# Kernel tuning notes

Measured on AMD Instinct MI355X. Metric: run time of the kernel, lower is better.

Reference implementation:

```python
import jax, jax.numpy as jnp
import numpy as np

N_WIRES = 4
N_REUP = 3
N_Q_LAYERS = 2
SEQ_LEN = 10
GRU_HIDDEN = 16


def setup_inputs() -> dict:
    key = jax.random.key(0)
    ks = jax.random.split(key, 24)
    N, E = 10000, 320000
    s = 0.25
    inp = {
        'x': jax.random.normal(ks[0], (N, SEQ_LEN + 3), jnp.float32),
        'edge_index': jax.random.randint(ks[1], (2, E), 0, N, dtype=jnp.int32),
        'edge_attr': jax.random.normal(ks[2], (E, 1), jnp.float32),
        'W_ih': jax.random.normal(ks[3], (3 * GRU_HIDDEN, 1), jnp.float32) * s,
        'W_hh': jax.random.normal(ks[4], (3 * GRU_HIDDEN, GRU_HIDDEN), jnp.float32) * s,
        'b_ih': jax.random.normal(ks[5], (3 * GRU_HIDDEN,), jnp.float32) * s,
        'b_hh': jax.random.normal(ks[6], (3 * GRU_HIDDEN,), jnp.float32) * s,
        'p1_W': jax.random.normal(ks[7], (N_WIRES, GRU_HIDDEN + 3), jnp.float32) * s,
        'p1_b': jax.random.normal(ks[8], (N_WIRES,), jnp.float32) * s,
        'a1_W': jax.random.normal(ks[9], (1, 2 * N_WIRES), jnp.float32) * s,
        'q1_w': jax.random.uniform(ks[10], (N_REUP, N_Q_LAYERS, 2), jnp.float32, -np.pi, np.pi),
        'g1': jnp.ones((N_WIRES,), jnp.float32),
        'be1': jnp.zeros((N_WIRES,), jnp.float32),
        'p2_W': jax.random.normal(ks[11], (N_WIRES, N_WIRES), jnp.float32) * s,
        'p2_b': jax.random.normal(ks[12], (N_WIRES,), jnp.float32) * s,
        'a2_W': jax.random.normal(ks[13], (1, 2 * N_WIRES), jnp.float32) * s,
        'q2_w': jax.random.uniform(ks[14], (N_REUP, N_Q_LAYERS, 2), jnp.float32, -np.pi, np.pi),
        'g2': jnp.ones((N_WIRES,), jnp.float32),
        'be2': jnp.zeros((N_WIRES,), jnp.float32),
        'r_W': jax.random.normal(ks[15], (1, N_WIRES), jnp.float32) * s,
        'r_b': jax.random.normal(ks[16], (1,), jnp.float32) * s,
    }
    return inp


def _ry(theta):
    c = jnp.cos(theta * 0.5)
    s = jnp.sin(theta * 0.5)
    return jnp.stack([jnp.stack([c, -s], -1), jnp.stack([s, c], -1)], -2).astype(jnp.complex64)


def _rz(theta):
    em = jnp.exp(-0.5j * theta)
    ep = jnp.exp(0.5j * theta)
    z = jnp.zeros_like(em)
    return jnp.stack([jnp.stack([em, z], -1), jnp.stack([z, ep], -1)], -2)


def _apply1q(state, gate, wire):
    # state: [E,2,2,2,2]; gate: [2,2] shared or [E,2,2] per-edge
    st = jnp.moveaxis(state, 1 + wire, -1)
    if gate.ndim == 3:
        st = jnp.einsum('eij,e...j->e...i', gate, st)
    else:
        st = jnp.einsum('ij,e...j->e...i', gate, st)
    return jnp.moveaxis(st, -1, 1 + wire)


def _cnot(state, c, t):
    st = jnp.moveaxis(state, (1 + c, 1 + t), (-2, -1))
    st = jnp.concatenate([st[..., :1, :], st[..., 1:, ::-1]], axis=-2)
    return jnp.moveaxis(st, (-2, -1), (1 + c, 1 + t))


def _qcircuit(inputs, corr, weights):
    # inputs: [E,4] angles, corr: [E], weights: [3,2,2]; batched 4-wire statevector sim
    E = inputs.shape[0]
    state = jnp.zeros((E, 16), jnp.complex64).at[:, 0].set(1.0).reshape(E, 2, 2, 2, 2)
    for r in range(N_REUP):
        for i in range(N_WIRES):
            state = _apply1q(state, _ry(inputs[:, i]), i)
        state = _apply1q(state, _ry(corr), 0)
        for d in range(N_Q_LAYERS):
            gy = _ry(weights[r, d, 0])
            gz = _rz(weights[r, d, 1])
            for i in range(N_WIRES):
                state = _apply1q(state, gy, i)
                state = _apply1q(state, gz, i)
            for i in range(d % 2, N_WIRES - 1, 2):
                state = _cnot(state, i, i + 1)
    probs = state.real ** 2 + state.imag ** 2
    z = jnp.array([1.0, -1.0], jnp.float32)
    return jnp.stack(
        [jnp.einsum('e...j,j->e', jnp.moveaxis(probs, 1 + w, -1), z) for w in range(N_WIRES)], -1)


def _layernorm(x, g, b):
    mu = x.mean(-1, keepdims=True)
    v = ((x - mu) ** 2).mean(-1, keepdims=True)
    return (x - mu) * jax.lax.rsqrt(v + 1e-5) * g + b


def _qgat(x, edge_index, edge_attr, Wp, bp, Wa, qw, g, b):
    N = x.shape[0]
    h = jax.nn.elu(x @ Wp.T + bp)  # [N,4]
    sl = jnp.arange(N, dtype=edge_index.dtype)
    src = jnp.concatenate([edge_index[0], sl])
    dst = jnp.concatenate([edge_index[1], sl])
    ea = jnp.concatenate([edge_attr[:, 0], jnp.ones((N,), x.dtype)])
    alpha = jnp.concatenate([h[src], h[dst]], -1) @ Wa[0]  # [Et]
    alpha = jax.nn.leaky_relu(alpha, 0.2) * jnp.abs(ea)
    alpha = alpha - jax.lax.stop_gradient(alpha).max()
    aexp = jnp.exp(alpha)
    dsum = jax.ops.segment_sum(aexp, dst, num_segments=N)
    alpha = aexp / (dsum[dst] + 1e-8)
    corr = jnp.tanh(ea) * jnp.pi
    msg = alpha[:, None] * _qcircuit(jnp.tanh(h[src]) * jnp.pi, corr, qw)  # [Et,4]
    aggr = jax.ops.segment_sum(msg, dst, num_segments=N)
    return _layernorm(aggr + h, g, b)


def _gru_last(price_seq, W_ih, W_hh, b_ih, b_hh):
    # price_seq: [N,T] scalar-per-step GRU; returns final hidden [N,H]
    N = price_seq.shape[0]
    h0 = jnp.zeros((N, GRU_HIDDEN), price_seq.dtype)
    w_in = W_ih[:, 0]  # [3H]

    def step(h, x_t):
        gi = x_t[:, None] * w_in + b_ih  # [N,3H]
        gh = h @ W_hh.T + b_hh
        ir, iz, inn = jnp.split(gi, 3, -1)
        hr, hz, hn = jnp.split(gh, 3, -1)
        r = jax.nn.sigmoid(ir + hr)
        z = jax.nn.sigmoid(iz + hz)
        n = jnp.tanh(inn + r * hn)
        return (1.0 - z) * n + z * h, None

    h, _ = jax.lax.scan(step, h0, price_seq.T)
    return h


def reference(x, edge_index, edge_attr, W_ih, W_hh, b_ih, b_hh,
              p1_W, p1_b, a1_W, q1_w, g1, be1,
              p2_W, p2_b, a2_W, q2_w, g2, be2, r_W, r_b):
    hT = _gru_last(x[:, :SEQ_LEN], W_ih, W_hh, b_ih, b_hh)
    h = jnp.concatenate([hT, x[:, SEQ_LEN:]], -1)  # [N,19]
    h = jax.nn.relu(_qgat(h, edge_index, edge_attr, p1_W, p1_b, a1_W, q1_w, g1, be1))
    h = _qgat(h, edge_index, edge_attr, p2_W, p2_b, a2_W, q2_w, g2, be2)
    return (h @ r_W.T + r_b)[:, 0]
```

## Files before the change

### kernel.cpp

```cpp
#include <hip/hip_runtime.h>
#include <math.h>


#define GH 16
#define SEQ 10
#define PI_F 3.14159265358979323846f

__device__ __forceinline__ float sigmoidf_(float x) { return 1.0f / (1.0f + expf(-x)); }

__global__ __launch_bounds__(256) void k_gru(
    const float* __restrict__ x, const float* __restrict__ W_ih,
    const float* __restrict__ W_hh, const float* __restrict__ b_ih,
    const float* __restrict__ b_hh, const float* __restrict__ p1W,
    const float* __restrict__ p1b, const float* __restrict__ a1W,
    const int* __restrict__ ei, int* __restrict__ deg,
    float* __restrict__ nrec1, float* __restrict__ hdd1,
    float* __restrict__ Sz, int N, int E)
{
    for (int i = blockIdx.x * 256 + threadIdx.x; i < N * 10; i += gridDim.x * 256)
        Sz[i] = 0.f;
    for (int e = blockIdx.x * 256 + threadIdx.x; e < E; e += gridDim.x * 256)
        atomicAdd(&deg[ei[E + e]], 1);

    __shared__ float sW[48 * 16];
    __shared__ float sp1W[4 * 19], sp1b[4];
    for (int i = threadIdx.x; i < 48 * 16; i += 256) sW[i] = W_hh[i];
    if (threadIdx.x < 76) sp1W[threadIdx.x] = p1W[threadIdx.x];
    if (threadIdx.x < 4) sp1b[threadIdx.x] = p1b[threadIdx.x];
    __syncthreads();

    const int j = threadIdx.x & 15;
    const int n = blockIdx.x * 16 + (threadIdx.x >> 4);
    const bool valid = (n < N);

    float wr[GH], wz[GH], wn[GH];
#pragma unroll
    for (int k = 0; k < GH; ++k) {
        wr[k] = sW[j * 16 + k];
        wz[k] = sW[(16 + j) * 16 + k];
        wn[k] = sW[(32 + j) * 16 + k];
    }
    float wir = W_ih[j], wiz = W_ih[16 + j], win_ = W_ih[32 + j];
    float bir = b_ih[j], biz = b_ih[16 + j], bin_ = b_ih[32 + j];
    float brr = b_hh[j], brz = b_hh[16 + j], brn = b_hh[32 + j];

    float xv[13];
#pragma unroll
    for (int t = 0; t < 13; ++t) xv[t] = valid ? x[n * 13 + t] : 0.f;

    float h = 0.f;
#pragma unroll
    for (int t = 0; t < SEQ; ++t) {
        float xt = xv[t];
        float ghr = brr, ghz = brz, ghn = brn;
#pragma unroll
        for (int k = 0; k < GH; ++k) {
            float hk = __shfl(h, k, 16);
            ghr += wr[k] * hk; ghz += wz[k] * hk; ghn += wn[k] * hk;
        }
        float r  = sigmoidf_(xt * wir + bir + ghr);
        float z  = sigmoidf_(xt * wiz + biz + ghz);
        float nv = tanhf(xt * win_ + bin_ + r * ghn);
        h = (1.f - z) * nv + z * h;
    }

    float s0 = h * sp1W[0 * 19 + j];
    float s1 = h * sp1W[1 * 19 + j];
    float s2 = h * sp1W[2 * 19 + j];
    float s3 = h * sp1W[3 * 19 + j];
#pragma unroll
    for (int m = 1; m < 16; m <<= 1) {
        s0 += __shfl_xor(s0, m, 16);
        s1 += __shfl_xor(s1, m, 16);
        s2 += __shfl_xor(s2, m, 16);
        s3 += __shfl_xor(s3, m, 16);
    }
    if (valid && j < 4) {
        float s = (j == 0) ? s0 : (j == 1) ? s1 : (j == 2) ? s2 : s3;
        s += sp1b[j] + xv[10] * sp1W[j * 19 + 16] + xv[11] * sp1W[j * 19 + 17]
           + xv[12] * sp1W[j * 19 + 18];
        float hv = (s > 0.f) ? s : expm1f(s);
        float* nb = nrec1 + (size_t)n * 16;
        float sv, cv; sincosf(0.5f * PI_F * tanhf(hv), &sv, &cv);
        nb[2 * j]     = cv;
        nb[2 * j + 1] = sv;
        nb[12 + j]    = hv;
        float ds = hv * a1W[j];
        float dd = hv * a1W[4 + j];
        ds += __shfl_xor(ds, 1); ds += __shfl_xor(ds, 2);
        dd += __shfl_xor(dd, 1); dd += __shfl_xor(dd, 2);
        if (j == 0) { nb[8] = ds; hdd1[n] = dd; }
    }
}

__global__ __launch_bounds__(1024) void k_scan(
    const int* __restrict__ deg, int* __restrict__ off,
    int* __restrict__ cur, int N)
{
    __shared__ int part[1024];
    const int t = threadIdx.x;
    const int chunk = (N + 1023) / 1024;
    const int lo = t * chunk;
    const int hi = min(lo + chunk, N);
    int s = 0;
    for (int i = lo; i < hi; ++i) s += deg[i] + 1;
    part[t] = s;
    __syncthreads();
    for (int d = 1; d < 1024; d <<= 1) {
        int y = (t >= d) ? part[t - d] : 0;
        __syncthreads();
        part[t] += y;
        __syncthreads();
    }
    int run = part[t] - s;
    for (int i = lo; i < hi; ++i) { off[i] = run; cur[i] = run; run += deg[i] + 1; }
}

__global__ __launch_bounds__(256) void k_fill(
    const int* __restrict__ ei, const float* __restrict__ ea,
    int* __restrict__ cur, float4* __restrict__ rec, int E, int N)
{
    int idx = blockIdx.x * 256 + threadIdx.x;
    if (idx >= E + N) return;
    int src, d; float ev;
    if (idx < E) { src = ei[idx]; d = ei[E + idx]; ev = ea[idx]; }
    else         { src = idx - E; d = src;         ev = 1.0f;    }
    int slot = atomicAdd(&cur[d], 1);
    float scv, ccv; sincosf(0.5f * PI_F * tanhf(ev), &scv, &ccv);
    float4 r;
    r.x = __int_as_float(src | (d << 16));
    r.y = fabsf(ev);
    r.z = ccv; r.w = scv;
    rec[slot] = r;
}

template <int STR>
__device__ __forceinline__ void ry_g(float (&sr)[16], float (&si)[16], float c, float s) {
#pragma unroll
    for (int i0 = 0; i0 < 16; ++i0) {
        if (i0 & STR) continue;
        int i1 = i0 | STR;
        float a0r = sr[i0], a0i = si[i0], a1r = sr[i1], a1i = si[i1];
        sr[i0] = c * a0r - s * a1r; si[i0] = c * a0i - s * a1i;
        sr[i1] = s * a0r + c * a1r; si[i1] = s * a0i + c * a1i;
    }
}
template <int STR>
__device__ __forceinline__ void rz_g(float (&sr)[16], float (&si)[16], float c, float s) {
#pragma unroll
    for (int i = 0; i < 16; ++i) {
        float r = sr[i], im = si[i];
        if (i & STR) { sr[i] = r * c - im * s; si[i] = im * c + r * s; }
        else         { sr[i] = r * c + im * s; si[i] = im * c - r * s; }
    }
}
template <int SC, int ST>
__device__ __forceinline__ void cnot_g(float (&sr)[16], float (&si)[16]) {
#pragma unroll
    for (int i = 0; i < 16; ++i) {
        if ((i & SC) && !(i & ST)) {
            int j = i | ST;
            float tr = sr[i], ti = si[i];
            sr[i] = sr[j]; si[i] = si[j]; sr[j] = tr; si[j] = ti;
        }
    }
}

__global__ __launch_bounds__(128) void k_gmat(
    const float* __restrict__ q1w, const float* __restrict__ q2w,
    float* __restrict__ Gtab)
{
    int t = threadIdx.x;
    if (t >= 96) return;
    int layer = t / 48, rem = t % 48, rep = rem / 16, col = rem % 16;
    const float* qw = layer ? q2w : q1w;
    float sr[16], si[16];
#pragma unroll
    for (int i = 0; i < 16; ++i) { sr[i] = 0.f; si[i] = 0.f; }
    sr[col] = 1.f;
#pragma unroll
    for (int d = 0; d < 2; ++d) {
        float cy, sy, cz, sz;
        sincosf(0.5f * qw[(rep * 2 + d) * 2 + 0], &sy, &cy);
        sincosf(0.5f * qw[(rep * 2 + d) * 2 + 1], &sz, &cz);
        bool lastd = (rep == 2) && (d == 1);
        ry_g<8>(sr, si, cy, sy); if (!lastd) rz_g<8>(sr, si, cz, sz);
        ry_g<4>(sr, si, cy, sy); if (!lastd) rz_g<4>(sr, si, cz, sz);
        ry_g<2>(sr, si, cy, sy); if (!lastd) rz_g<2>(sr, si, cz, sz);
        ry_g<1>(sr, si, cy, sy); if (!lastd) rz_g<1>(sr, si, cz, sz);
        if (d == 0) { cnot_g<8, 4>(sr, si); cnot_g<2, 1>(sr, si); }
        else        { cnot_g<4, 2>(sr, si); }
    }
    float* g = Gtab + layer * 1536 + rep * 512;
#pragma unroll
    for (int i = 0; i < 16; ++i) {
        g[(i * 16 + col) * 2 + 0] = sr[i];
        g[(i * 16 + col) * 2 + 1] = si[i];
    }
}

__global__ __launch_bounds__(256) void k_prep(
    const float* __restrict__ nrec, const float* __restrict__ Gl,
    float* __restrict__ T, int N)
{
    __shared__ float gr[3][16 * 17], gi[3][16 * 17];
    for (int idx = threadIdx.x; idx < 3 * 256; idx += 256) {
        int rep = idx >> 8, rc = idx & 255, i = rc >> 4, jj = rc & 15;
        gr[rep][i * 17 + jj] = Gl[rep * 512 + rc * 2 + 0];
        gi[rep][i * 17 + jj] = Gl[rep * 512 + rc * 2 + 1];
    }
    __syncthreads();

    const int lane = threadIdx.x & 15;
    const int n = blockIdx.x * 16 + (threadIdx.x >> 4);
    if (n >= N) return;
    const float* nb = nrec + (size_t)n * 16;
    const float c1 = nb[2], s1 = nb[3], c2 = nb[4], s2 = nb[5], c3 = nb[6], s3 = nb[7];

    float pa = (lane & 8) ? 0.f
             : ((lane & 4) ? s1 : c1) * ((lane & 2) ? s2 : c2) * ((lane & 1) ? s3 : c3);
    float pb;
    { float t = __shfl_xor(pa, 8, 16); pb = (lane & 8) ? t : -t; }

    float ar = 0.f, ai = 0.f, br = 0.f, bi = 0.f;
#pragma unroll
    for (int jj = 0; jj < 16; ++jj) {
        float Gr = gr[0][lane * 17 + jj], Gi = gi[0][lane * 17 + jj];
        float xa = __shfl(pa, jj, 16), xb = __shfl(pb, jj, 16);
        ar += Gr * xa; ai += Gi * xa; br += Gr * xb; bi += Gi * xb;
    }

#define BFLY(vr, vi, STR, cc, ss) { \
    float tr_ = __shfl_xor(vr, STR, 16), ti_ = __shfl_xor(vi, STR, 16); \
    float sg_ = (lane & STR) ? (ss) : -(ss); \
    vr = (cc) * vr + sg_ * tr_; vi = (cc) * vi + sg_ * ti_; }
#define R123(vr, vi) { BFLY(vr, vi, 4, c1, s1) BFLY(vr, vi, 2, c2, s2) BFLY(vr, vi, 1, c3, s3) }
#define KAPP(orr, oii, xr, xi) { \
    float tr_ = __shfl_xor(xr, 8, 16), ti_ = __shfl_xor(xi, 8, 16); \
    orr = (lane & 8) ? tr_ : -tr_; oii = (lane & 8) ? ti_ : -ti_; }

    R123(ar, ai) R123(br, bi)

    float sr4[4], si4[4];
    sr4[0] = ar; si4[0] = ai;
    KAPP(sr4[1], si4[1], ar, ai)
    sr4[2] = br; si4[2] = bi;
    KAPP(sr4[3], si4[3], br, bi)

    float nr4[4] = {0.f, 0.f, 0.f, 0.f}, ni4[4] = {0.f, 0.f, 0.f, 0.f};
#pragma unroll
    for (int jj = 0; jj < 16; ++jj) {
        float Gr = gr[1][lane * 17 + jj], Gi = gi[1][lane * 17 + jj];
#pragma unroll
        for (int v = 0; v < 4; ++v) {
            float xr = __shfl(sr4[v], jj, 16), xi = __shfl(si4[v], jj, 16);
            nr4[v] += Gr * xr - Gi * xi;
            ni4[v] += Gr * xi + Gi * xr;
        }
    }
#pragma unroll
    for (int v = 0; v < 4; ++v) { R123(nr4[v], ni4[v]) }

    float gr4[4], gi4[4];
    float m01r = nr4[1] + nr4[2], m01i = ni4[1] + ni4[2];
    gr4[0] = nr4[0]; gi4[0] = ni4[0];
    { float kr, ki; KAPP(kr, ki, nr4[0], ni4[0]) gr4[1] = m01r + kr; gi4[1] = m01i + ki; }
    { float kr, ki; KAPP(kr, ki, m01r, m01i)     gr4[2] = nr4[3] + kr; gi4[2] = ni4[3] + ki; }
    { float kr, ki; KAPP(kr, ki, nr4[3], ni4[3]) gr4[3] = kr; gi4[3] = ki; }

    float vr4[4] = {0.f, 0.f, 0.f, 0.f}, vi4[4] = {0.f, 0.f, 0.f, 0.f};
#pragma unroll
    for (int jj = 0; jj < 16; ++jj) {
        float Gr = gr[2][lane * 17 + jj], Gi = gi[2][lane * 17 + jj];
#pragma unroll
        for (int v = 0; v < 4; ++v) {
            float xr = __shfl(gr4[v], jj, 16), xi = __shfl(gi4[v], jj, 16);
            vr4[v] += Gr * xr - Gi * xi;
            vi4[v] += Gr * xi + Gi * xr;
        }
    }

    float p[10];
    {
        int idx = 0;
#pragma unroll
        for (int k = 0; k < 4; ++k)
#pragma unroll
            for (int l = 0; l < 4; ++l) {
                if (l < k) continue;
                p[idx++] = vr4[k] * vr4[l] + vi4[k] * vi4[l];
            }
    }
#pragma unroll
    for (int pi = 0; pi < 10; ++pi) {
        float v = p[pi];
#pragma unroll
        for (int m = 8; m >= 1; m >>= 1) {
            float t = __shfl_xor(v, m, 16);
            v = (lane & m) ? (t - v) : (v + t);
        }
        p[pi] = v;
    }

    float* Tb = T + (size_t)n * 48;
    int w = (lane == 8) ? 0 : (lane == 4) ? 1 : (lane == 2) ? 2 : (lane == 1) ? 3 : -1;
    if (w >= 0) {
#pragma unroll
        for (int pi = 0; pi < 10; ++pi) {
            float mult = (pi == 0 || pi == 4 || pi == 7 || pi == 9) ? 1.f : 2.f;
            Tb[w * 10 + pi] = mult * p[pi];
        }
    }
    if (lane == 0) { Tb[40] = nb[0]; Tb[41] = nb[1]; Tb[42] = nb[8]; Tb[43] = 0.f; }
#undef BFLY
#undef R123
#undef KAPP
}

__device__ __forceinline__ void segreduce(
    int dst, int lane, float a0, float a1, float a2, float a3, float a4,
    float* __restrict__ S)
{
    int prevd = __shfl_up(dst, 1);
    bool head = (lane == 0) || (prevd != dst);
    unsigned long long hm = __ballot(head);
    unsigned long long below = (2ull << lane) - 1ull;
    int H = 63 - __clzll((long long)(hm & below));
    int dist = lane - H;
#pragma unroll
    for (int st = 1; st < 64; st <<= 1) {
        float t0 = __shfl_up(a0, st), t1 = __shfl_up(a1, st),
              t2 = __shfl_up(a2, st), t3 = __shfl_up(a3, st),
              t4 = __shfl_up(a4, st);
        if (dist >= st) { a0 += t0; a1 += t1; a2 += t2; a3 += t3; a4 += t4; }
    }
    int nextd = __shfl_down(dst, 1);
    bool lastl = (lane == 63) || (dst != nextd);
    if (lastl && dst >= 0) {
        float* sbase = S + (size_t)dst * 5;
        atomicAdd(sbase + 0, a0); atomicAdd(sbase + 1, a1);
        atomicAdd(sbase + 2, a2); atomicAdd(sbase + 3, a3);
        atomicAdd(sbase + 4, a4);
    }
}

__global__ __launch_bounds__(256) void k_edge(
    const float4* __restrict__ rec, const float* __restrict__ T,
    const float* __restrict__ hdd, float* __restrict__ S, int EN)
{
    const int slot = blockIdx.x * 256 + threadIdx.x;
    const int lane = threadIdx.x & 63;
    int dst = -1;
    float acc0 = 0.f, acc1 = 0.f, acc2 = 0.f, acc3 = 0.f, acc4 = 0.f;

    if (slot < EN) {
        float4 r = rec[slot];
        int ids = __float_as_int(r.x);
        int src = ids & 0xFFFF;
        dst = ids >> 16;
        float aea = r.y, ccv = r.z, scv = r.w;

        const float* Tb = T + (size_t)src * 48;
        float t[44];
#pragma unroll
        for (int q = 0; q < 11; ++q) {
            float4 v4 = *reinterpret_cast<const float4*>(Tb + q * 4);
            t[q * 4 + 0] = v4.x; t[q * 4 + 1] = v4.y;
            t[q * 4 + 2] = v4.z; t[q * 4 + 3] = v4.w;
        }
        float hdN = hdd[dst];

        float mc = t[40] * ccv - t[41] * scv;
        float ms = t[41] * ccv + t[40] * scv;
        float m2 = mc * mc, s2 = ms * ms;
        float cf0 = mc * m2, cf1 = m2 * ms, cf2 = mc * s2, cf3 = ms * s2;
        float qq[10];
        qq[0] = cf0 * cf0; qq[1] = cf0 * cf1; qq[2] = cf0 * cf2; qq[3] = cf0 * cf3;
        qq[4] = cf1 * cf1; qq[5] = cf1 * cf2; qq[6] = cf1 * cf3;
        qq[7] = cf2 * cf2; qq[8] = cf2 * cf3; qq[9] = cf3 * cf3;

        float z0 = 0.f, z1 = 0.f, z2 = 0.f, z3 = 0.f;
#pragma unroll
        for (int pi = 0; pi < 10; ++pi) {
            z0 += t[pi] * qq[pi];
            z1 += t[10 + pi] * qq[pi];
            z2 += t[20 + pi] * qq[pi];
            z3 += t[30 + pi] * qq[pi];
        }

        float s0a = t[42] + hdN;
        s0a = (s0a > 0.f) ? s0a : 0.2f * s0a;
        float aexp = expf(s0a * aea);
        acc0 = aexp * z0; acc1 = aexp * z1; acc2 = aexp * z2; acc3 = aexp * z3;
        acc4 = aexp;
    }
    segreduce(dst, lane, acc0, acc1, acc2, acc3, acc4, S);
}

template <bool FINAL>
__global__ __launch_bounds__(256) void k_node(
    const float* __restrict__ S, const float* __restrict__ nrec,
    const float* __restrict__ g4, const float* __restrict__ be4,
    const float* __restrict__ pW, const float* __restrict__ pb,
    const float* __restrict__ WaN, const float* __restrict__ rW,
    const float* __restrict__ rb, float* __restrict__ onrec,
    float* __restrict__ ohdd, float* __restrict__ out, int N)
{
    int n = blockIdx.x * 256 + threadIdx.x;
    if (n >= N) return;
    const float* sb = S + (size_t)n * 5;
    const float* nb = nrec + (size_t)n * 16;
    float dn = sb[4] + 1e-8f;
    float v0 = sb[0] / dn + nb[12];
    float v1 = sb[1] / dn + nb[13];
    float v2 = sb[2] / dn + nb[14];
    float v3 = sb[3] / dn + nb[15];
    float mu = 0.25f * (v0 + v1 + v2 + v3);
    float d0 = v0 - mu, d1 = v1 - mu, d2 = v2 - mu, d3 = v3 - mu;
    float var = 0.25f * (d0 * d0 + d1 * d1 + d2 * d2 + d3 * d3);
    float rs = 1.0f / sqrtf(var + 1e-5f);
    float y0 = d0 * rs * g4[0] + be4[0];
    float y1 = d1 * rs * g4[1] + be4[1];
    float y2 = d2 * rs * g4[2] + be4[2];
    float y3 = d3 * rs * g4[3] + be4[3];

    if (FINAL) {
        out[n] = rb[0] + y0 * rW[0] + y1 * rW[1] + y2 * rW[2] + y3 * rW[3];
    } else {
        y0 = fmaxf(y0, 0.f); y1 = fmaxf(y1, 0.f);
        y2 = fmaxf(y2, 0.f); y3 = fmaxf(y3, 0.f);
        float hv[4];
#pragma unroll
        for (int w = 0; w < 4; ++w) {
            float s = pb[w] + y0 * pW[w * 4 + 0] + y1 * pW[w * 4 + 1]
                    + y2 * pW[w * 4 + 2] + y3 * pW[w * 4 + 3];
            hv[w] = (s > 0.f) ? s : expm1f(s);
        }
        float* ob = onrec + (size_t)n * 16;
        float ds = 0.f, dd = 0.f;
#pragma unroll
        for (int w = 0; w < 4; ++w) {
            float sv, cv; sincosf(0.5f * PI_F * tanhf(hv[w]), &sv, &cv);
            ob[2 * w]     = cv;
            ob[2 * w + 1] = sv;
            ob[12 + w]    = hv[w];
            ds += hv[w] * WaN[w];
            dd += hv[w] * WaN[4 + w];
        }
        ob[8] = ds;
        ohdd[n] = dd;
    }
}

extern "C" void kernel_launch(void* const* d_in, const int* in_sizes, int n_in,
                              void* d_out, int out_size, void* d_ws, size_t ws_size,
                              hipStream_t stream)
{
    const float* x    = (const float*)d_in[0];
    const int*   ei   = (const int*)d_in[1];
    const float* ea   = (const float*)d_in[2];
    const float* W_ih = (const float*)d_in[3];
    const float* W_hh = (const float*)d_in[4];
    const float* b_ih = (const float*)d_in[5];
    const float* b_hh = (const float*)d_in[6];
    const float* p1W  = (const float*)d_in[7];
    const float* p1b  = (const float*)d_in[8];
    const float* a1W  = (const float*)d_in[9];
    const float* q1w  = (const float*)d_in[10];
    const float* g1   = (const float*)d_in[11];
    const float* be1  = (const float*)d_in[12];
    const float* p2W  = (const float*)d_in[13];
    const float* p2b  = (const float*)d_in[14];
    const float* a2W  = (const float*)d_in[15];
    const float* q2w  = (const float*)d_in[16];
    const float* g2   = (const float*)d_in[17];
    const float* be2  = (const float*)d_in[18];
    const float* rW   = (const float*)d_in[19];
    const float* rb   = (const float*)d_in[20];
    float* out = (float*)d_out;

    int N  = in_sizes[0] / 13;
    int E  = in_sizes[1] / 2;
    int EN = E + N;

    float* ws    = (float*)d_ws;
    float* nrec1 = ws;
    float* nrec2 = nrec1 + (size_t)N * 16;
    float* hdd1  = nrec2 + (size_t)N * 16;
    float* hdd2  = hdd1 + N;
    float* S1    = hdd2 + N;
    float* S2    = S1 + (size_t)N * 5;
    float* Gtab  = S2 + (size_t)N * 5;
    float* T     = Gtab + 3072;
    int* deg  = (int*)(T + (size_t)N * 48);
    int* off  = deg + N;
    int* cur  = off + N;
    uintptr_t rp = (uintptr_t)(cur + N);
    rp = (rp + 15u) & ~(uintptr_t)15u;
    float4* rec = (float4*)rp;

    hipMemsetAsync(deg, 0, (size_t)N * sizeof(int), stream);

    const int B = 256;
    k_gru<<<(N + 15) / 16, B, 0, stream>>>(x, W_ih, W_hh, b_ih, b_hh, p1W, p1b,
                                           a1W, ei, deg, nrec1, hdd1, S1, N, E);
    k_scan<<<1, 1024, 0, stream>>>(deg, off, cur, N);
    k_fill<<<(EN + B - 1) / B, B, 0, stream>>>(ei, ea, cur, rec, E, N);
    k_gmat<<<1, 128, 0, stream>>>(q1w, q2w, Gtab);

    k_prep<<<(N + 15) / 16, B, 0, stream>>>(nrec1, Gtab, T, N);
    k_edge<<<(EN + B - 1) / B, B, 0, stream>>>(rec, T, hdd1, S1, EN);
    k_node<false><<<(N + B - 1) / B, B, 0, stream>>>(
        S1, nrec1, g1, be1, p2W, p2b, a2W, rW, rb, nrec2, hdd2, out, N);

    k_prep<<<(N + 15) / 16, B, 0, stream>>>(nrec2, Gtab + 1536, T, N);
    k_edge<<<(EN + B - 1) / B, B, 0, stream>>>(rec, T, hdd2, S2, EN);
    k_node<true><<<(N + B - 1) / B, B, 0, stream>>>(
        S2, nrec2, g2, be2, p2W, p2b, a2W, rW, rb, nrec2, hdd2, out, N);
}
```

Baseline: 238.3 us.

## Fuse per-node quantum prep into GRU and node-update kernels

Moves the per-node quantum-circuit preparation (k_prep) into the GRU kernel for layer 1 and into the node-update kernel for layer 2. This removes two kernel launches and the round trip through the 16-float node record, which shrinks to a 4-float residual buffer. k_gmat now runs before the GRU so the fused kernel can load the gate tables. The cost is that the node-update work now runs at 16 lanes per node with redundant math, and the GRU kernel carries more shared memory and registers.

```diff
diff --git a/kernel.cpp b/kernel.cpp
--- a/kernel.cpp
+++ b/kernel.cpp
@@ -7,14 +7,186 @@
 #define PI_F 3.14159265358979323846f
 
 __device__ __forceinline__ float sigmoidf_(float x) { return 1.0f / (1.0f + expf(-x)); }
+
+template <int STR>
+__device__ __forceinline__ void ry_g(float (&sr)[16], float (&si)[16], float c, float s) {
+#pragma unroll
+    for (int i0 = 0; i0 < 16; ++i0) {
+        if (i0 & STR) continue;
+        int i1 = i0 | STR;
+        float a0r = sr[i0], a0i = si[i0], a1r = sr[i1], a1i = si[i1];
+        sr[i0] = c * a0r - s * a1r; si[i0] = c * a0i - s * a1i;
+        sr[i1] = s * a0r + c * a1r; si[i1] = s * a0i + c * a1i;
+    }
+}
+template <int STR>
+__device__ __forceinline__ void rz_g(float (&sr)[16], float (&si)[16], float c, float s) {
+#pragma unroll
+    for (int i = 0; i < 16; ++i) {
+        float r = sr[i], im = si[i];
+        if (i & STR) { sr[i] = r * c - im * s; si[i] = im * c + r * s; }
+        else         { sr[i] = r * c + im * s; si[i] = im * c - r * s; }
+    }
+}
+template <int SC, int ST>
+__device__ __forceinline__ void cnot_g(float (&sr)[16], float (&si)[16]) {
+#pragma unroll
+    for (int i = 0; i < 16; ++i) {
+        if ((i & SC) && !(i & ST)) {
+            int j = i | ST;
+            float tr = sr[i], ti = si[i];
+            sr[i] = sr[j]; si[i] = si[j]; sr[j] = tr; si[j] = ti;
+        }
+    }
+}
+
+__global__ __launch_bounds__(128) void k_gmat(
+    const float* __restrict__ q1w, const float* __restrict__ q2w,
+    float* __restrict__ Gtab)
+{
+    int t = threadIdx.x;
+    if (t >= 96) return;
+    int layer = t / 48, rem = t % 48, rep = rem / 16, col = rem % 16;
+    const float* qw = layer ? q2w : q1w;
+    float sr[16], si[16];
+#pragma unroll
+    for (int i = 0; i < 16; ++i) { sr[i] = 0.f; si[i] = 0.f; }
+    sr[col] = 1.f;
+#pragma unroll
+    for (int d = 0; d < 2; ++d) {
+        float cy, sy, cz, sz;
+        sincosf(0.5f * qw[(rep * 2 + d) * 2 + 0], &sy, &cy);
+        sincosf(0.5f * qw[(rep * 2 + d) * 2 + 1], &sz, &cz);
+        bool lastd = (rep == 2) && (d == 1);
+        ry_g<8>(sr, si, cy, sy); if (!lastd) rz_g<8>(sr, si, cz, sz);
+        ry_g<4>(sr, si, cy, sy); if (!lastd) rz_g<4>(sr, si, cz, sz);
+        ry_g<2>(sr, si, cy, sy); if (!lastd) rz_g<2>(sr, si, cz, sz);
+        ry_g<1>(sr, si, cy, sy); if (!lastd) rz_g<1>(sr, si, cz, sz);
+        if (d == 0) { cnot_g<8, 4>(sr, si); cnot_g<2, 1>(sr, si); }
+        else        { cnot_g<4, 2>(sr, si); }
+    }
+    float* g = Gtab + layer * 1536 + rep * 512;
+#pragma unroll
+    for (int i = 0; i < 16; ++i) {
+        g[(i * 16 + col) * 2 + 0] = sr[i];
+        g[(i * 16 + col) * 2 + 1] = si[i];
+    }
+}
+
+__device__ __forceinline__ void prep_node(
+    int lane, int n, float c0, float s0, float c1, float s1,
+    float c2, float s2, float c3, float s3, float hsd,
+    const float (&gr)[3][16 * 17], const float (&gi)[3][16 * 17],
+    float* __restrict__ T)
+{
+    float pa = (lane & 8) ? 0.f
+             : ((lane & 4) ? s1 : c1) * ((lane & 2) ? s2 : c2) * ((lane & 1) ? s3 : c3);
+    float pb;
+    { float t = __shfl_xor(pa, 8, 16); pb = (lane & 8) ? t : -t; }
+
+    float ar = 0.f, ai = 0.f, br = 0.f, bi = 0.f;
+#pragma unroll
+    for (int jj = 0; jj < 16; ++jj) {
+        float Gr = gr[0][lane * 17 + jj], Gi = gi[0][lane * 17 + jj];
+        float xa = __shfl(pa, jj, 16), xb = __shfl(pb, jj, 16);
+        ar += Gr * xa; ai += Gi * xa; br += Gr * xb; bi += Gi * xb;
+    }
+
+#define BFLY(vr, vi, STR, cc, ss) { \
+    float tr_ = __shfl_xor(vr, STR, 16), ti_ = __shfl_xor(vi, STR, 16); \
+    float sg_ = (lane & STR) ? (ss) : -(ss); \
+    vr = (cc) * vr + sg_ * tr_; vi = (cc) * vi + sg_ * ti_; }
+#define R123(vr, vi) { BFLY(vr, vi, 4, c1, s1) BFLY(vr, vi, 2, c2, s2) BFLY(vr, vi, 1, c3, s3) }
+#define KAPP(orr, oii, xr, xi) { \
+    float tr_ = __shfl_xor(xr, 8, 16), ti_ = __shfl_xor(xi, 8, 16); \
+    orr = (lane & 8) ? tr_ : -tr_; oii = (lane & 8) ? ti_ : -ti_; }
+
+    R123(ar, ai) R123(br, bi)
+
+    float sr4[4], si4[4];
+    sr4[0] = ar; si4[0] = ai;
+    KAPP(sr4[1], si4[1], ar, ai)
+    sr4[2] = br; si4[2] = bi;
+    KAPP(sr4[3], si4[3], br, bi)
+
+    float nr4[4] = {0.f, 0.f, 0.f, 0.f}, ni4[4] = {0.f, 0.f, 0.f, 0.f};
+#pragma unroll
+    for (int jj = 0; jj < 16; ++jj) {
+        float Gr = gr[1][lane * 17 + jj], Gi = gi[1][lane * 17 + jj];
+#pragma unroll
+        for (int v = 0; v < 4; ++v) {
+            float xr = __shfl(sr4[v], jj, 16), xi = __shfl(si4[v], jj, 16);
+            nr4[v] += Gr * xr - Gi * xi;
+            ni4[v] += Gr * xi + Gi * xr;
+        }
+    }
+#pragma unroll
+    for (int v = 0; v < 4; ++v) { R123(nr4[v], ni4[v]) }
+
+    float gr4[4], gi4[4];
+    float m01r = nr4[1] + nr4[2], m01i = ni4[1] + ni4[2];
+    gr4[0] = nr4[0]; gi4[0] = ni4[0];
+    { float kr, ki; KAPP(kr, ki, nr4[0], ni4[0]) gr4[1] = m01r + kr; gi4[1] = m01i + ki; }
+    { float kr, ki; KAPP(kr, ki, m01r, m01i)     gr4[2] = nr4[3] + kr; gi4[2] = ni4[3] + ki; }
+    { float kr, ki; KAPP(kr, ki, nr4[3], ni4[3]) gr4[3] = kr; gi4[3] = ki; }
+
+    float vr4[4] = {0.f, 0.f, 0.f, 0.f}, vi4[4] = {0.f, 0.f, 0.f, 0.f};
+#pragma unroll
+    for (int jj = 0; jj < 16; ++jj) {
+        float Gr = gr[2][lane * 17 + jj], Gi = gi[2][lane * 17 + jj];
+#pragma unroll
+        for (int v = 0; v < 4; ++v) {
+            float xr = __shfl(gr4[v], jj, 16), xi = __shfl(gi4[v], jj, 16);
+            vr4[v] += Gr * xr - Gi * xi;
+            vi4[v] += Gr * xi + Gi * xr;
+        }
+    }
+
+    float p[10];
+    {
+        int idx = 0;
+#pragma unroll
+        for (int k = 0; k < 4; ++k)
+#pragma unroll
+            for (int l = 0; l < 4; ++l) {
+                if (l < k) continue;
+                p[idx++] = vr4[k] * vr4[l] + vi4[k] * vi4[l];
+            }
+    }
+#pragma unroll
+    for (int pi = 0; pi < 10; ++pi) {
+        float v = p[pi];
+#pragma unroll
+        for (int m = 8; m >= 1; m >>= 1) {
+            float t = __shfl_xor(v, m, 16);
+            v = (lane & m) ? (t - v) : (v + t);
+        }
+        p[pi] = v;
+    }
+
+    float* Tb = T + (size_t)n * 48;
+    int w = (lane == 8) ? 0 : (lane == 4) ? 1 : (lane == 2) ? 2 : (lane == 1) ? 3 : -1;
+    if (w >= 0) {
+#pragma unroll
+        for (int pi = 0; pi < 10; ++pi) {
+            float mult = (pi == 0 || pi == 4 || pi == 7 || pi == 9) ? 1.f : 2.f;
+            Tb[w * 10 + pi] = mult * p[pi];
+        }
+    }
+    if (lane == 0) { Tb[40] = c0; Tb[41] = s0; Tb[42] = hsd; Tb[43] = 0.f; }
+#undef BFLY
+#undef R123
+#undef KAPP
+}
 
 __global__ __launch_bounds__(256) void k_gru(
     const float* __restrict__ x, const float* __restrict__ W_ih,
     const float* __restrict__ W_hh, const float* __restrict__ b_ih,
     const float* __restrict__ b_hh, const float* __restrict__ p1W,
     const float* __restrict__ p1b, const float* __restrict__ a1W,
-    const int* __restrict__ ei, int* __restrict__ deg,
-    float* __restrict__ nrec1, float* __restrict__ hdd1,
+    const float* __restrict__ Gl, const int* __restrict__ ei,
+    int* __restrict__ deg, float* __restrict__ nres1,
+    float* __restrict__ hdd1, float* __restrict__ T,
     float* __restrict__ Sz, int N, int E)
 {
     for (int i = blockIdx.x * 256 + threadIdx.x; i < N * 10; i += gridDim.x * 256)
@@ -24,9 +196,15 @@
 
     __shared__ float sW[48 * 16];
     __shared__ float sp1W[4 * 19], sp1b[4];
+    __shared__ float gr[3][16 * 17], gi[3][16 * 17];
     for (int i = threadIdx.x; i < 48 * 16; i += 256) sW[i] = W_hh[i];
     if (threadIdx.x < 76) sp1W[threadIdx.x] = p1W[threadIdx.x];
     if (threadIdx.x < 4) sp1b[threadIdx.x] = p1b[threadIdx.x];
+    for (int idx = threadIdx.x; idx < 3 * 256; idx += 256) {
+        int rep = idx >> 8, rc = idx & 255, i = rc >> 4, jj = rc & 15;
+        gr[rep][i * 17 + jj] = Gl[rep * 512 + rc * 2 + 0];
+        gi[rep][i * 17 + jj] = Gl[rep * 512 + rc * 2 + 1];
+    }
     __syncthreads();
 
     const int j = threadIdx.x & 15;
@@ -64,32 +242,41 @@
         h = (1.f - z) * nv + z * h;
     }
 
-    float s0 = h * sp1W[0 * 19 + j];
-    float s1 = h * sp1W[1 * 19 + j];
-    float s2 = h * sp1W[2 * 19 + j];
-    float s3 = h * sp1W[3 * 19 + j];
+    float b0 = h * sp1W[0 * 19 + j];
+    float b1 = h * sp1W[1 * 19 + j];
+    float b2 = h * sp1W[2 * 19 + j];
+    float b3 = h * sp1W[3 * 19 + j];
 #pragma unroll
     for (int m = 1; m < 16; m <<= 1) {
-        s0 += __shfl_xor(s0, m, 16);
-        s1 += __shfl_xor(s1, m, 16);
-        s2 += __shfl_xor(s2, m, 16);
-        s3 += __shfl_xor(s3, m, 16);
-    }
-    if (valid && j < 4) {
-        float s = (j == 0) ? s0 : (j == 1) ? s1 : (j == 2) ? s2 : s3;
+        b0 += __shfl_xor(b0, m, 16);
+        b1 += __shfl_xor(b1, m, 16);
+        b2 += __shfl_xor(b2, m, 16);
+        b3 += __shfl_xor(b3, m, 16);
+    }
+
+    float hv = 0.f, cv = 1.f, sv = 0.f, ds = 0.f, dd = 0.f;
+    if (j < 4) {
+        float s = (j == 0) ? b0 : (j == 1) ? b1 : (j == 2) ? b2 : b3;
         s += sp1b[j] + xv[10] * sp1W[j * 19 + 16] + xv[11] * sp1W[j * 19 + 17]
            + xv[12] * sp1W[j * 19 + 18];
-        float hv = (s > 0.f) ? s : expm1f(s);
-        float* nb = nrec1 + (size_t)n * 16;
-        float sv, cv; sincosf(0.5f * PI_F * tanhf(hv), &sv, &cv);
-        nb[2 * j]     = cv;
-        nb[2 * j + 1] = sv;
-        nb[12 + j]    = hv;
-        float ds = hv * a1W[j];
-        float dd = hv * a1W[4 + j];
-        ds += __shfl_xor(ds, 1); ds += __shfl_xor(ds, 2);
-        dd += __shfl_xor(dd, 1); dd += __shfl_xor(dd, 2);
-        if (j == 0) { nb[8] = ds; hdd1[n] = dd; }
+        hv = (s > 0.f) ? s : expm1f(s);
+        sincosf(0.5f * PI_F * tanhf(hv), &sv, &cv);
+        ds = hv * a1W[j];
+        dd = hv * a1W[4 + j];
+    }
+    ds += __shfl_xor(ds, 1, 16); ds += __shfl_xor(ds, 2, 16);
+    dd += __shfl_xor(dd, 1, 16); dd += __shfl_xor(dd, 2, 16);
+
+    float c0 = __shfl(cv, 0, 16), s0 = __shfl(sv, 0, 16);
+    float c1 = __shfl(cv, 1, 16), s1 = __shfl(sv, 1, 16);
+    float c2 = __shfl(cv, 2, 16), s2 = __shfl(sv, 2, 16);
+    float c3 = __shfl(cv, 3, 16), s3 = __shfl(sv, 3, 16);
+    float hsd = __shfl(ds, 0, 16);
+
+    if (valid) {
+        if (j < 4) nres1[n * 4 + j] = hv;
+        if (j == 0) hdd1[n] = dd;
+        prep_node(j, n, c0, s0, c1, s1, c2, s2, c3, s3, hsd, gr, gi, T);
     }
 }
 
@@ -134,189 +321,6 @@
     rec[slot] = r;
 }
 
-template <int STR>
-__device__ __forceinline__ void ry_g(float (&sr)[16], float (&si)[16], float c, float s) {
-#pragma unroll
-    for (int i0 = 0; i0 < 16; ++i0) {
-        if (i0 & STR) continue;
-        int i1 = i0 | STR;
-        float a0r = sr[i0], a0i = si[i0], a1r = sr[i1], a1i = si[i1];
-        sr[i0] = c * a0r - s * a1r; si[i0] = c * a0i - s * a1i;
-        sr[i1] = s * a0r + c * a1r; si[i1] = s * a0i + c * a1i;
-    }
-}
-template <int STR>
-__device__ __forceinline__ void rz_g(float (&sr)[16], float (&si)[16], float c, float s) {
-#pragma unroll
-    for (int i = 0; i < 16; ++i) {
-        float r = sr[i], im = si[i];
-        if (i & STR) { sr[i] = r * c - im * s; si[i] = im * c + r * s; }
-        else         { sr[i] = r * c + im * s; si[i] = im * c - r * s; }
-    }
-}
-template <int SC, int ST>
-__device__ __forceinline__ void cnot_g(float (&sr)[16], float (&si)[16]) {
-#pragma unroll
-    for (int i = 0; i < 16; ++i) {
-        if ((i & SC) && !(i & ST)) {
-            int j = i | ST;
-            float tr = sr[i], ti = si[i];
-            sr[i] = sr[j]; si[i] = si[j]; sr[j] = tr; si[j] = ti;
-        }
-    }
-}
-
-__global__ __launch_bounds__(128) void k_gmat(
-    const float* __restrict__ q1w, const float* __restrict__ q2w,
-    float* __restrict__ Gtab)
-{
-    int t = threadIdx.x;
-    if (t >= 96) return;
-    int layer = t / 48, rem = t % 48, rep = rem / 16, col = rem % 16;
-    const float* qw = layer ? q2w : q1w;
-    float sr[16], si[16];
-#pragma unroll
-    for (int i = 0; i < 16; ++i) { sr[i] = 0.f; si[i] = 0.f; }
-    sr[col] = 1.f;
-#pragma unroll
-    for (int d = 0; d < 2; ++d) {
-        float cy, sy, cz, sz;
-        sincosf(0.5f * qw[(rep * 2 + d) * 2 + 0], &sy, &cy);
-        sincosf(0.5f * qw[(rep * 2 + d) * 2 + 1], &sz, &cz);
-        bool lastd = (rep == 2) && (d == 1);
-        ry_g<8>(sr, si, cy, sy); if (!lastd) rz_g<8>(sr, si, cz, sz);
-        ry_g<4>(sr, si, cy, sy); if (!lastd) rz_g<4>(sr, si, cz, sz);
-        ry_g<2>(sr, si, cy, sy); if (!lastd) rz_g<2>(sr, si, cz, sz);
-        ry_g<1>(sr, si, cy, sy); if (!lastd) rz_g<1>(sr, si, cz, sz);
-        if (d == 0) { cnot_g<8, 4>(sr, si); cnot_g<2, 1>(sr, si); }
-        else        { cnot_g<4, 2>(sr, si); }
-    }
-    float* g = Gtab + layer * 1536 + rep * 512;
-#pragma unroll
-    for (int i = 0; i < 16; ++i) {
-        g[(i * 16 + col) * 2 + 0] = sr[i];
-        g[(i * 16 + col) * 2 + 1] = si[i];
-    }
-}
-
-__global__ __launch_bounds__(256) void k_prep(
-    const float* __restrict__ nrec, const float* __restrict__ Gl,
-    float* __restrict__ T, int N)
-{
-    __shared__ float gr[3][16 * 17], gi[3][16 * 17];
-    for (int idx = threadIdx.x; idx < 3 * 256; idx += 256) {
-        int rep = idx >> 8, rc = idx & 255, i = rc >> 4, jj = rc & 15;
-        gr[rep][i * 17 + jj] = Gl[rep * 512 + rc * 2 + 0];
-        gi[rep][i * 17 + jj] = Gl[rep * 512 + rc * 2 + 1];
-    }
-    __syncthreads();
-
-    const int lane = threadIdx.x & 15;
-    const int n = blockIdx.x * 16 + (threadIdx.x >> 4);
-    if (n >= N) return;
-    const float* nb = nrec + (size_t)n * 16;
-    const float c1 = nb[2], s1 = nb[3], c2 = nb[4], s2 = nb[5], c3 = nb[6], s3 = nb[7];
-
-    float pa = (lane & 8) ? 0.f
-             : ((lane & 4) ? s1 : c1) * ((lane & 2) ? s2 : c2) * ((lane & 1) ? s3 : c3);
-    float pb;
-    { float t = __shfl_xor(pa, 8, 16); pb = (lane & 8) ? t : -t; }
-
-    float ar = 0.f, ai = 0.f, br = 0.f, bi = 0.f;
-#pragma unroll
-    for (int jj = 0; jj < 16; ++jj) {
-        float Gr = gr[0][lane * 17 + jj], Gi = gi[0][lane * 17 + jj];
-        float xa = __shfl(pa, jj, 16), xb = __shfl(pb, jj, 16);
-        ar += Gr * xa; ai += Gi * xa; br += Gr * xb; bi += Gi * xb;
-    }
-
-#define BFLY(vr, vi, STR, cc, ss) { \
-    float tr_ = __shfl_xor(vr, STR, 16), ti_ = __shfl_xor(vi, STR, 16); \
-    float sg_ = (lane & STR) ? (ss) : -(ss); \
-    vr = (cc) * vr + sg_ * tr_; vi = (cc) * vi + sg_ * ti_; }
-#define R123(vr, vi) { BFLY(vr, vi, 4, c1, s1) BFLY(vr, vi, 2, c2, s2) BFLY(vr, vi, 1, c3, s3) }
-#define KAPP(orr, oii, xr, xi) { \
-    float tr_ = __shfl_xor(xr, 8, 16), ti_ = __shfl_xor(xi, 8, 16); \
-    orr = (lane & 8) ? tr_ : -tr_; oii = (lane & 8) ? ti_ : -ti_; }
-
-    R123(ar, ai) R123(br, bi)
-
-    float sr4[4], si4[4];
-    sr4[0] = ar; si4[0] = ai;
-    KAPP(sr4[1], si4[1], ar, ai)
-    sr4[2] = br; si4[2] = bi;
-    KAPP(sr4[3], si4[3], br, bi)
-
-    float nr4[4] = {0.f, 0.f, 0.f, 0.f}, ni4[4] = {0.f, 0.f, 0.f, 0.f};
-#pragma unroll
-    for (int jj = 0; jj < 16; ++jj) {
-        float Gr = gr[1][lane * 17 + jj], Gi = gi[1][lane * 17 + jj];
-#pragma unroll
-        for (int v = 0; v < 4; ++v) {
-            float xr = __shfl(sr4[v], jj, 16), xi = __shfl(si4[v], jj, 16);
-            nr4[v] += Gr * xr - Gi * xi;
-            ni4[v] += Gr * xi + Gi * xr;
-        }
-    }
-#pragma unroll
-    for (int v = 0; v < 4; ++v) { R123(nr4[v], ni4[v]) }
-
-    float gr4[4], gi4[4];
-    float m01r = nr4[1] + nr4[2], m01i = ni4[1] + ni4[2];
-    gr4[0] = nr4[0]; gi4[0] = ni4[0];
-    { float kr, ki; KAPP(kr, ki, nr4[0], ni4[0]) gr4[1] = m01r + kr; gi4[1] = m01i + ki; }
-    { float kr, ki; KAPP(kr, ki, m01r, m01i)     gr4[2] = nr4[3] + kr; gi4[2] = ni4[3] + ki; }
-    { float kr, ki; KAPP(kr, ki, nr4[3], ni4[3]) gr4[3] = kr; gi4[3] = ki; }
-
-    float vr4[4] = {0.f, 0.f, 0.f, 0.f}, vi4[4] = {0.f, 0.f, 0.f, 0.f};
-#pragma unroll
-    for (int jj = 0; jj < 16; ++jj) {
-        float Gr = gr[2][lane * 17 + jj], Gi = gi[2][lane * 17 + jj];
-#pragma unroll
-        for (int v = 0; v < 4; ++v) {
-            float xr = __shfl(gr4[v], jj, 16), xi = __shfl(gi4[v], jj, 16);
-            vr4[v] += Gr * xr - Gi * xi;
-            vi4[v] += Gr * xi + Gi * xr;
-        }
-    }
-
-    float p[10];
-    {
-        int idx = 0;
-#pragma unroll
-        for (int k = 0; k < 4; ++k)
-#pragma unroll
-            for (int l = 0; l < 4; ++l) {
-                if (l < k) continue;
-                p[idx++] = vr4[k] * vr4[l] + vi4[k] * vi4[l];
-            }
-    }
-#pragma unroll
-    for (int pi = 0; pi < 10; ++pi) {
-        float v = p[pi];
-#pragma unroll
-        for (int m = 8; m >= 1; m >>= 1) {
-            float t = __shfl_xor(v, m, 16);
-            v = (lane & m) ? (t - v) : (v + t);
-        }
-        p[pi] = v;
-    }
-
-    float* Tb = T + (size_t)n * 48;
-    int w = (lane == 8) ? 0 : (lane == 4) ? 1 : (lane == 2) ? 2 : (lane == 1) ? 3 : -1;
-    if (w >= 0) {
-#pragma unroll
-        for (int pi = 0; pi < 10; ++pi) {
-            float mult = (pi == 0 || pi == 4 || pi == 7 || pi == 9) ? 1.f : 2.f;
-            Tb[w * 10 + pi] = mult * p[pi];
-        }
-    }
-    if (lane == 0) { Tb[40] = nb[0]; Tb[41] = nb[1]; Tb[42] = nb[8]; Tb[43] = 0.f; }
-#undef BFLY
-#undef R123
-#undef KAPP
-}
-
 __device__ __forceinline__ void segreduce(
     int dst, int lane, float a0, float a1, float a2, float a3, float a4,
     float* __restrict__ S)
@@ -397,59 +401,87 @@
     segreduce(dst, lane, acc0, acc1, acc2, acc3, acc4, S);
 }
 
-template <bool FINAL>
-__global__ __launch_bounds__(256) void k_node(
-    const float* __restrict__ S, const float* __restrict__ nrec,
+__global__ __launch_bounds__(256) void k_nodeprep(
+    const float* __restrict__ S, const float* __restrict__ nres,
     const float* __restrict__ g4, const float* __restrict__ be4,
     const float* __restrict__ pW, const float* __restrict__ pb,
-    const float* __restrict__ WaN, const float* __restrict__ rW,
-    const float* __restrict__ rb, float* __restrict__ onrec,
-    float* __restrict__ ohdd, float* __restrict__ out, int N)
-{
-    int n = blockIdx.x * 256 + threadIdx.x;
+    const float* __restrict__ WaN, const float* __restrict__ Gl,
+    float* __restrict__ onres, float* __restrict__ ohdd,
+    float* __restrict__ T, int N)
+{
+    __shared__ float gr[3][16 * 17], gi[3][16 * 17];
+    for (int idx = threadIdx.x; idx < 3 * 256; idx += 256) {
+        int rep = idx >> 8, rc = idx & 255, i = rc >> 4, jj = rc & 15;
+        gr[rep][i * 17 + jj] = Gl[rep * 512 + rc * 2 + 0];
+        gi[rep][i * 17 + jj] = Gl[rep * 512 + rc * 2 + 1];
+    }
+    __syncthreads();
+
+    const int lane = threadIdx.x & 15;
+    const int n = blockIdx.x * 16 + (threadIdx.x >> 4);
     if (n >= N) return;
+
     const float* sb = S + (size_t)n * 5;
-    const float* nb = nrec + (size_t)n * 16;
     float dn = sb[4] + 1e-8f;
-    float v0 = sb[0] / dn + nb[12];
-    float v1 = sb[1] / dn + nb[13];
-    float v2 = sb[2] / dn + nb[14];
-    float v3 = sb[3] / dn + nb[15];
+    float v0 = sb[0] / dn + nres[n * 4 + 0];
+    float v1 = sb[1] / dn + nres[n * 4 + 1];
+    float v2 = sb[2] / dn + nres[n * 4 + 2];
+    float v3 = sb[3] / dn + nres[n * 4 + 3];
     float mu = 0.25f * (v0 + v1 + v2 + v3);
     float d0 = v0 - mu, d1 = v1 - mu, d2 = v2 - mu, d3 = v3 - mu;
     float var = 0.25f * (d0 * d0 + d1 * d1 + d2 * d2 + d3 * d3);
     float rs = 1.0f / sqrtf(var + 1e-5f);
-    float y0 = d0 * rs * g4[0] + be4[0];
-    float y1 = d1 * rs * g4[1] + be4[1];
-    float y2 = d2 * rs * g4[2] + be4[2];
-    float y3 = d3 * rs * g4[3] + be4[3];
-
-    if (FINAL) {
-        out[n] = rb[0] + y0 * rW[0] + y1 * rW[1] + y2 * rW[2] + y3 * rW[3];
-    } else {
-        y0 = fmaxf(y0, 0.f); y1 = fmaxf(y1, 0.f);
-        y2 = fmaxf(y2, 0.f); y3 = fmaxf(y3, 0.f);
-        float hv[4];
-#pragma unroll
-        for (int w = 0; w < 4; ++w) {
-            float s = pb[w] + y0 * pW[w * 4 + 0] + y1 * pW[w * 4 + 1]
-                    + y2 * pW[w * 4 + 2] + y3 * pW[w * 4 + 3];
-            hv[w] = (s > 0.f) ? s : expm1f(s);
-        }
-        float* ob = onrec + (size_t)n * 16;
-        float ds = 0.f, dd = 0.f;
-#pragma unroll
-        for (int w = 0; w < 4; ++w) {
-            float sv, cv; sincosf(0.5f * PI_F * tanhf(hv[w]), &sv, &cv);
-            ob[2 * w]     = cv;
-            ob[2 * w + 1] = sv;
-            ob[12 + w]    = hv[w];
-            ds += hv[w] * WaN[w];
-            dd += hv[w] * WaN[4 + w];
-        }
-        ob[8] = ds;
-        ohdd[n] = dd;
-    }
+    float y0 = fmaxf(d0 * rs * g4[0] + be4[0], 0.f);
+    float y1 = fmaxf(d1 * rs * g4[1] + be4[1], 0.f);
+    float y2 = fmaxf(d2 * rs * g4[2] + be4[2], 0.f);
+    float y3 = fmaxf(d3 * rs * g4[3] + be4[3], 0.f);
+
+    float hv[4];
+#pragma unroll
+    for (int w = 0; w < 4; ++w) {
+        float s = pb[w] + y0 * pW[w * 4 + 0] + y1 * pW[w * 4 + 1]
+                + y2 * pW[w * 4 + 2] + y3 * pW[w * 4 + 3];
+        hv[w] = (s > 0.f) ? s : expm1f(s);
+    }
+
+    float cv = 1.f, sv = 0.f;
+    if (lane < 4) sincosf(0.5f * PI_F * tanhf(hv[lane]), &sv, &cv);
+    float c0 = __shfl(cv, 0, 16), s0 = __shfl(sv, 0, 16);
+    float c1 = __shfl(cv, 1, 16), s1 = __shfl(sv, 1, 16);
+    float c2 = __shfl(cv, 2, 16), s2 = __shfl(sv, 2, 16);
+    float c3 = __shfl(cv, 3, 16), s3 = __shfl(sv, 3, 16);
+
+    float hsd = hv[0] * WaN[0] + hv[1] * WaN[1] + hv[2] * WaN[2] + hv[3] * WaN[3];
+    if (lane < 4) onres[n * 4 + lane] = hv[lane];
+    if (lane == 0)
+        ohdd[n] = hv[0] * WaN[4] + hv[1] * WaN[5] + hv[2] * WaN[6] + hv[3] * WaN[7];
+
+    prep_node(lane, n, c0, s0, c1, s1, c2, s2, c3, s3, hsd, gr, gi, T);
+}
+
+__global__ __launch_bounds__(256) void k_node2(
+    const float* __restrict__ S, const float* __restrict__ nres,
+    const float* __restrict__ g4, const float* __restrict__ be4,
+    const float* __restrict__ rW, const float* __restrict__ rb,
+    float* __restrict__ out, int N)
+{
+    int n = blockIdx.x * 256 + threadIdx.x;
+    if (n >= N) return;
+    const float* sb = S + (size_t)n * 5;
+    float dn = sb[4] + 1e-8f;
+    float v0 = sb[0] / dn + nres[n * 4 + 0];
+    float v1 = sb[1] / dn + nres[n * 4 + 1];
+    float v2 = sb[2] / dn + nres[n * 4 + 2];
+    float v3 = sb[3] / dn + nres[n * 4 + 3];
+    float mu = 0.25f * (v0 + v1 + v2 + v3);
+    float d0 = v0 - mu, d1 = v1 - mu, d2 = v2 - mu, d3 = v3 - mu;
+    float var = 0.25f * (d0 * d0 + d1 * d1 + d2 * d2 + d3 * d3);
+    float rs = 1.0f / sqrtf(var + 1e-5f);
+    out[n] = rb[0]
+           + (d0 * rs * g4[0] + be4[0]) * rW[0]
+           + (d1 * rs * g4[1] + be4[1]) * rW[1]
+           + (d2 * rs * g4[2] + be4[2]) * rW[2]
+           + (d3 * rs * g4[3] + be4[3]) * rW[3];
 }
 
 extern "C" void kernel_launch(void* const* d_in, const int* in_sizes, int n_in,
@@ -484,9 +516,9 @@
     int EN = E + N;
 
     float* ws    = (float*)d_ws;
-    float* nrec1 = ws;
-    float* nrec2 = nrec1 + (size_t)N * 16;
-    float* hdd1  = nrec2 + (size_t)N * 16;
+    float* nres1 = ws;
+    float* nres2 = nres1 + (size_t)N * 4;
+    float* hdd1  = nres2 + (size_t)N * 4;
     float* hdd2  = hdd1 + N;
     float* S1    = hdd2 + N;
     float* S2    = S1 + (size_t)N * 5;
@@ -502,19 +534,17 @@
     hipMemsetAsync(deg, 0, (size_t)N * sizeof(int), stream);
 
     const int B = 256;
+    k_gmat<<<1, 128, 0, stream>>>(q1w, q2w, Gtab);
     k_gru<<<(N + 15) / 16, B, 0, stream>>>(x, W_ih, W_hh, b_ih, b_hh, p1W, p1b,
-                                           a1W, ei, deg, nrec1, hdd1, S1, N, E);
+                                           a1W, Gtab, ei, deg, nres1, hdd1, T,
+                                           S1, N, E);
     k_scan<<<1, 1024, 0, stream>>>(deg, off, cur, N);
     k_fill<<<(EN + B - 1) / B, B, 0, stream>>>(ei, ea, cur, rec, E, N);
-    k_gmat<<<1, 128, 0, stream>>>(q1w, q2w, Gtab);
-
-    k_prep<<<(N + 15) / 16, B, 0, stream>>>(nrec1, Gtab, T, N);
+
     k_edge<<<(EN + B - 1) / B, B, 0, stream>>>(rec, T, hdd1, S1, EN);
-    k_node<false><<<(N + B - 1) / B, B, 0, stream>>>(
-        S1, nrec1, g1, be1, p2W, p2b, a2W, rW, rb, nrec2, hdd2, out, N);
-
-    k_prep<<<(N + 15) / 16, B, 0, stream>>>(nrec2, Gtab + 1536, T, N);
+    k_nodeprep<<<(N + 15) / 16, B, 0, stream>>>(
+        S1, nres1, g1, be1, p2W, p2b, a2W, Gtab + 1536, nres2, hdd2, T, N);
+
     k_edge<<<(EN + B - 1) / B, B, 0, stream>>>(rec, T, hdd2, S2, EN);
-    k_node<true><<<(N + B - 1) / B, B, 0, stream>>>(
-        S2, nrec2, g2, be2, p2W, p2b, a2W, rW, rb, nrec2, hdd2, out, N);
-}
+    k_node2<<<(N + B - 1) / B, B, 0, stream>>>(S2, nres2, g2, be2, rW, rb, out, N);
+}
```

New measurement: 232.8 us. 1.02x faster.
